# Kernel tuning notes

Measured on AMD Instinct MI355X. Metric: run time of the kernel, lower is better.

## Reference

```python
import jax, jax.numpy as jnp
import numpy as np

B, N = 32, 4096
EMBED_DIM = 256
D = H = W = 64


def setup_inputs() -> dict:
    key = jax.random.key(0)
    k1, k2, k3, k4 = jax.random.split(key, 4)
    points = jax.random.uniform(k1, (B, N, 3), dtype=jnp.float32) * D  # coords in [0, image_size)
    labels = jax.random.randint(k2, (B, N), 0, 2, dtype=jnp.int32)
    pos_embed = jax.random.normal(k3, (1, EMBED_DIM, D, H, W), dtype=jnp.float32) * 0.02
    point_emb = jax.random.normal(k4, (2, EMBED_DIM), dtype=jnp.float32)
    return {"points": points, "labels": labels, "pos_embed": pos_embed, "point_emb": point_emb}


def reference(points, labels, pos_embed, point_emb):
    # int() truncation (coords are non-negative) then clamp to grid bounds
    idx = jnp.clip(points.astype(jnp.int32), 0, jnp.array([D - 1, H - 1, W - 1], dtype=jnp.int32))
    zi, yi, xi = idx[..., 0], idx[..., 1], idx[..., 2]  # each [B, N]
    grid = jnp.transpose(pos_embed[0], (1, 2, 3, 0))  # [D, H, W, C]
    pos_enc = grid[zi, yi, xi]                        # [B, N, C] vectorized gather
    type_emb = point_emb[labels]                      # [B, N, C]
    return pos_enc + type_emb
```

## Files before the change

### kernel.cpp

```cpp
#include <hip/hip_runtime.h>


constexpr int B_ = 32;
constexpr int N_ = 4096;
constexpr int C_ = 256;
constexpr int GD = 64;
constexpr int PTS = B_ * N_;
constexpr int CELLS = GD * GD * GD;
constexpr int NBINS = GD * GD * (GD / 16);
constexpr int BPB = 8;
constexpr int NBLK = NBINS / BPB;
constexpr int TP = 260;

typedef float f32x4 __attribute__((ext_vector_type(4)));

__device__ __forceinline__ int clamp63(float v) {
    int i = (int)v;
    return min(max(i, 0), GD - 1);
}

__global__ __launch_bounds__(256) void k_zero(unsigned* __restrict__ hist) {
    int t = blockIdx.x * blockDim.x + threadIdx.x;
    if (t < NBINS) hist[t] = 0u;
}

__global__ __launch_bounds__(256) void k_hist(const float* __restrict__ points,
                                              unsigned* __restrict__ hist) {
    int p = blockIdx.x * blockDim.x + threadIdx.x;
    if (p >= PTS) return;
    int zi = clamp63(points[p * 3 + 0]);
    int yi = clamp63(points[p * 3 + 1]);
    int xi = clamp63(points[p * 3 + 2]);
    int key = (zi << 8) | (yi << 2) | (xi >> 4);
    atomicAdd(&hist[key], 1u);
}

__global__ __launch_bounds__(1024) void k_scan(const unsigned* __restrict__ hist,
                                               unsigned* __restrict__ cursor,
                                               unsigned* __restrict__ bin_ofs) {
    __shared__ unsigned sums[1024];
    const int t = threadIdx.x;
    unsigned h[16];
    unsigned s = 0;
    #pragma unroll
    for (int i = 0; i < 16; ++i) { h[i] = hist[t * 16 + i]; s += h[i]; }
    sums[t] = s;
    __syncthreads();
    for (int off = 1; off < 1024; off <<= 1) {
        unsigned v = (t >= off) ? sums[t - off] : 0u;
        __syncthreads();
        sums[t] += v;
        __syncthreads();
    }
    unsigned run = (t > 0) ? sums[t - 1] : 0u;
    #pragma unroll
    for (int i = 0; i < 16; ++i) {
        cursor[t * 16 + i]  = run;
        bin_ofs[t * 16 + i] = run;
        run += h[i];
    }
    if (t == 1023) bin_ofs[NBINS] = sums[1023];
}

__global__ __launch_bounds__(256) void k_scatter(const float* __restrict__ points,
                                                 const int* __restrict__ labels,
                                                 unsigned* __restrict__ cursor,
                                                 unsigned* __restrict__ recs) {
    int p = blockIdx.x * blockDim.x + threadIdx.x;
    if (p >= PTS) return;
    int zi = clamp63(points[p * 3 + 0]);
    int yi = clamp63(points[p * 3 + 1]);
    int xi = clamp63(points[p * 3 + 2]);
    int key = (zi << 8) | (yi << 2) | (xi >> 4);
    unsigned slot = atomicAdd(&cursor[key], 1u);
    recs[slot] = (unsigned)p | ((unsigned)labels[p] << 17) | ((unsigned)(xi & 15) << 18);
}

__global__ __launch_bounds__(256) void k_gather(const unsigned* __restrict__ bin_ofs,
                                                const unsigned* __restrict__ recs,
                                                const float* __restrict__ pos,
                                                const float* __restrict__ pemb,
                                                float* __restrict__ out) {
    __shared__ float tile[2][16 * TP];

    const int b    = blockIdx.x;
    const int swz  = (b & 7) * (NBLK >> 3) + (b >> 3);
    const int bin0 = swz * BPB;

    const int tid = threadIdx.x;
    const int w   = tid >> 6;
    const int l   = tid & 63;
    const int o4  = (tid & 3) << 2;
    const int csub = tid >> 2;

    const float4 te0 = *reinterpret_cast<const float4*>(pemb + 4 * l);
    const float4 te1 = *reinterpret_cast<const float4*>(pemb + C_ + 4 * l);

    auto linebase = [](int bin) -> size_t {
        return ((size_t)(bin >> 8) << 12) | ((size_t)((bin >> 2) & 63) << 6) |
               ((size_t)(bin & 3) << 4);
    };

    float4 rv0, rv1, rv2, rv3;
    {
        const size_t lb = linebase(bin0);
        rv0 = *reinterpret_cast<const float4*>(pos + (size_t)(  0 + csub) * CELLS + lb + o4);
        rv1 = *reinterpret_cast<const float4*>(pos + (size_t)( 64 + csub) * CELLS + lb + o4);
        rv2 = *reinterpret_cast<const float4*>(pos + (size_t)(128 + csub) * CELLS + lb + o4);
        rv3 = *reinterpret_cast<const float4*>(pos + (size_t)(192 + csub) * CELLS + lb + o4);
        float* t0 = tile[0];
        t0[(o4 + 0) * TP +   0 + csub] = rv0.x; t0[(o4 + 1) * TP +   0 + csub] = rv0.y;
        t0[(o4 + 2) * TP +   0 + csub] = rv0.z; t0[(o4 + 3) * TP +   0 + csub] = rv0.w;
        t0[(o4 + 0) * TP +  64 + csub] = rv1.x; t0[(o4 + 1) * TP +  64 + csub] = rv1.y;
        t0[(o4 + 2) * TP +  64 + csub] = rv1.z; t0[(o4 + 3) * TP +  64 + csub] = rv1.w;
        t0[(o4 + 0) * TP + 128 + csub] = rv2.x; t0[(o4 + 1) * TP + 128 + csub] = rv2.y;
        t0[(o4 + 2) * TP + 128 + csub] = rv2.z; t0[(o4 + 3) * TP + 128 + csub] = rv2.w;
        t0[(o4 + 0) * TP + 192 + csub] = rv3.x; t0[(o4 + 1) * TP + 192 + csub] = rv3.y;
        t0[(o4 + 2) * TP + 192 + csub] = rv3.z; t0[(o4 + 3) * TP + 192 + csub] = rv3.w;
    }

    for (int k = 0; k < BPB; ++k) {
        const int cur = k & 1;
        if (k + 1 < BPB) {
            const size_t lb = linebase(bin0 + k + 1);
            rv0 = *reinterpret_cast<const float4*>(pos + (size_t)(  0 + csub) * CELLS + lb + o4);
            rv1 = *reinterpret_cast<const float4*>(pos + (size_t)( 64 + csub) * CELLS + lb + o4);
            rv2 = *reinterpret_cast<const float4*>(pos + (size_t)(128 + csub) * CELLS + lb + o4);
            rv3 = *reinterpret_cast<const float4*>(pos + (size_t)(192 + csub) * CELLS + lb + o4);
        }
        __syncthreads();

        const int bin = bin0 + k;
        const unsigned start = bin_ofs[bin];
        const unsigned end   = bin_ofs[bin + 1];
        const float* tcur = tile[cur];
        for (unsigned i = start + w; i < end; i += 4) {
            const unsigned rec = recs[i];
            const unsigned p   = rec & 0x1FFFFu;
            const unsigned o   = rec >> 18;
            const float4 te = ((rec >> 17) & 1u) ? te1 : te0;
            const float4 v  = *reinterpret_cast<const float4*>(tcur + o * TP + 4 * l);
            f32x4 rr;
            rr.x = v.x + te.x; rr.y = v.y + te.y; rr.z = v.z + te.z; rr.w = v.w + te.w;
            __builtin_nontemporal_store(rr,
                reinterpret_cast<f32x4*>(out + (size_t)p * C_ + 4 * l));
        }

        if (k + 1 < BPB) {
            float* tn = tile[cur ^ 1];
            tn[(o4 + 0) * TP +   0 + csub] = rv0.x; tn[(o4 + 1) * TP +   0 + csub] = rv0.y;
            tn[(o4 + 2) * TP +   0 + csub] = rv0.z; tn[(o4 + 3) * TP +   0 + csub] = rv0.w;
            tn[(o4 + 0) * TP +  64 + csub] = rv1.x; tn[(o4 + 1) * TP +  64 + csub] = rv1.y;
            tn[(o4 + 2) * TP +  64 + csub] = rv1.z; tn[(o4 + 3) * TP +  64 + csub] = rv1.w;
            tn[(o4 + 0) * TP + 128 + csub] = rv2.x; tn[(o4 + 1) * TP + 128 + csub] = rv2.y;
            tn[(o4 + 2) * TP + 128 + csub] = rv2.z; tn[(o4 + 3) * TP + 128 + csub] = rv2.w;
            tn[(o4 + 0) * TP + 192 + csub] = rv3.x; tn[(o4 + 1) * TP + 192 + csub] = rv3.y;
            tn[(o4 + 2) * TP + 192 + csub] = rv3.z; tn[(o4 + 3) * TP + 192 + csub] = rv3.w;
        }
    }
}

__global__ __launch_bounds__(256) void k_naive(const float* __restrict__ points,
                                               const int* __restrict__ labels,
                                               const float* __restrict__ pos,
                                               const float* __restrict__ pemb,
                                               float* __restrict__ out) {
    const int t    = blockIdx.x * blockDim.x + threadIdx.x;
    const int p    = t >> 6;
    const int lane = t & 63;
    const int c4   = lane << 2;
    if (p >= PTS) return;
    int zi = clamp63(points[p * 3 + 0]);
    int yi = clamp63(points[p * 3 + 1]);
    int xi = clamp63(points[p * 3 + 2]);
    const int cell = (zi << 12) | (yi << 6) | xi;
    const int lab  = labels[p];
    const float4 te = *reinterpret_cast<const float4*>(pemb + lab * C_ + c4);
    const float* g = pos + cell;
    float4 r;
    r.x = g[(c4 + 0) * CELLS] + te.x;
    r.y = g[(c4 + 1) * CELLS] + te.y;
    r.z = g[(c4 + 2) * CELLS] + te.z;
    r.w = g[(c4 + 3) * CELLS] + te.w;
    *reinterpret_cast<float4*>(out + p * C_ + c4) = r;
}

extern "C" void kernel_launch(void* const* d_in, const int* in_sizes, int n_in,
                              void* d_out, int out_size, void* d_ws, size_t ws_size,
                              hipStream_t stream) {
    const float* points = (const float*)d_in[0];
    const int*   labels = (const int*)d_in[1];
    const float* pos    = (const float*)d_in[2];
    const float* pemb   = (const float*)d_in[3];
    float*       out    = (float*)d_out;

    const size_t need = (size_t)(NBINS * 3 + 1 + PTS) * sizeof(unsigned);
    if (ws_size < need) {
        const int total = PTS * 64;
        k_naive<<<(total + 255) / 256, 256, 0, stream>>>(points, labels, pos, pemb, out);
        return;
    }
    unsigned* hist    = (unsigned*)d_ws;
    unsigned* cursor  = hist + NBINS;
    unsigned* bin_ofs = cursor + NBINS;
    unsigned* recs    = bin_ofs + NBINS + 1;

    k_zero<<<(NBINS + 255) / 256, 256, 0, stream>>>(hist);
    k_hist<<<(PTS + 255) / 256, 256, 0, stream>>>(points, hist);
    k_scan<<<1, 1024, 0, stream>>>(hist, cursor, bin_ofs);
    k_scatter<<<(PTS + 255) / 256, 256, 0, stream>>>(points, labels, cursor, recs);
    k_gather<<<NBLK, 256, 0, stream>>>(bin_ofs, recs, pos, pemb, out);
}
```

Baseline: 108.8 us.

## Replace histogram+scan binning with fixed-capacity bins and overflow fallback

Drops the histogram, prefix-scan and second scatter pass, and bins points directly into fixed-capacity slots of 64 per bin with a single atomic pass. Points that overflow a bin are written directly by the scatter thread with a scalar per-channel loop. The zeroing kernel is replaced by a memset. This removes two kernel launches, the serial single-block scan and one full read of the points, at the cost of a larger, sparser record buffer. With the expected 2 points per bin on average, overflow should essentially never occur.

```diff
diff --git a/kernel.cpp b/kernel.cpp
--- a/kernel.cpp
+++ b/kernel.cpp
@@ -8,6 +8,7 @@
 constexpr int PTS = B_ * N_;
 constexpr int CELLS = GD * GD * GD;
 constexpr int NBINS = GD * GD * (GD / 16);
+constexpr int CAP = 64;
 constexpr int BPB = 8;
 constexpr int NBLK = NBINS / BPB;
 constexpr int TP = 260;
@@ -19,64 +20,32 @@
     return min(max(i, 0), GD - 1);
 }
 
-__global__ __launch_bounds__(256) void k_zero(unsigned* __restrict__ hist) {
-    int t = blockIdx.x * blockDim.x + threadIdx.x;
-    if (t < NBINS) hist[t] = 0u;
-}
-
-__global__ __launch_bounds__(256) void k_hist(const float* __restrict__ points,
-                                              unsigned* __restrict__ hist) {
+__global__ __launch_bounds__(256) void k_scatter(const float* __restrict__ points,
+                                                 const int* __restrict__ labels,
+                                                 unsigned* __restrict__ counts,
+                                                 unsigned* __restrict__ recs,
+                                                 const float* __restrict__ pos,
+                                                 const float* __restrict__ pemb,
+                                                 float* __restrict__ out) {
     int p = blockIdx.x * blockDim.x + threadIdx.x;
     if (p >= PTS) return;
     int zi = clamp63(points[p * 3 + 0]);
     int yi = clamp63(points[p * 3 + 1]);
     int xi = clamp63(points[p * 3 + 2]);
     int key = (zi << 8) | (yi << 2) | (xi >> 4);
-    atomicAdd(&hist[key], 1u);
+    int lab = labels[p];
+    unsigned slot = atomicAdd(&counts[key], 1u);
+    if (slot < CAP) {
+        recs[key * CAP + slot] =
+            (unsigned)p | ((unsigned)lab << 17) | ((unsigned)(xi & 15) << 18);
+    } else {
+        const int cell = (zi << 12) | (yi << 6) | xi;
+        for (int c = 0; c < C_; ++c)
+            out[(size_t)p * C_ + c] = pos[(size_t)c * CELLS + cell] + pemb[lab * C_ + c];
+    }
 }
 
-__global__ __launch_bounds__(1024) void k_scan(const unsigned* __restrict__ hist,
-                                               unsigned* __restrict__ cursor,
-                                               unsigned* __restrict__ bin_ofs) {
-    __shared__ unsigned sums[1024];
-    const int t = threadIdx.x;
-    unsigned h[16];
-    unsigned s = 0;
-    #pragma unroll
-    for (int i = 0; i < 16; ++i) { h[i] = hist[t * 16 + i]; s += h[i]; }
-    sums[t] = s;
-    __syncthreads();
-    for (int off = 1; off < 1024; off <<= 1) {
-        unsigned v = (t >= off) ? sums[t - off] : 0u;
-        __syncthreads();
-        sums[t] += v;
-        __syncthreads();
-    }
-    unsigned run = (t > 0) ? sums[t - 1] : 0u;
-    #pragma unroll
-    for (int i = 0; i < 16; ++i) {
-        cursor[t * 16 + i]  = run;
-        bin_ofs[t * 16 + i] = run;
-        run += h[i];
-    }
-    if (t == 1023) bin_ofs[NBINS] = sums[1023];
-}
-
-__global__ __launch_bounds__(256) void k_scatter(const float* __restrict__ points,
-                                                 const int* __restrict__ labels,
-                                                 unsigned* __restrict__ cursor,
-                                                 unsigned* __restrict__ recs) {
-    int p = blockIdx.x * blockDim.x + threadIdx.x;
-    if (p >= PTS) return;
-    int zi = clamp63(points[p * 3 + 0]);
-    int yi = clamp63(points[p * 3 + 1]);
-    int xi = clamp63(points[p * 3 + 2]);
-    int key = (zi << 8) | (yi << 2) | (xi >> 4);
-    unsigned slot = atomicAdd(&cursor[key], 1u);
-    recs[slot] = (unsigned)p | ((unsigned)labels[p] << 17) | ((unsigned)(xi & 15) << 18);
-}
-
-__global__ __launch_bounds__(256) void k_gather(const unsigned* __restrict__ bin_ofs,
+__global__ __launch_bounds__(256) void k_gather(const unsigned* __restrict__ counts,
                                                 const unsigned* __restrict__ recs,
                                                 const float* __restrict__ pos,
                                                 const float* __restrict__ pemb,
@@ -87,10 +56,10 @@
     const int swz  = (b & 7) * (NBLK >> 3) + (b >> 3);
     const int bin0 = swz * BPB;
 
-    const int tid = threadIdx.x;
-    const int w   = tid >> 6;
-    const int l   = tid & 63;
-    const int o4  = (tid & 3) << 2;
+    const int tid  = threadIdx.x;
+    const int w    = tid >> 6;
+    const int l    = tid & 63;
+    const int o4   = (tid & 3) << 2;
     const int csub = tid >> 2;
 
     const float4 te0 = *reinterpret_cast<const float4*>(pemb + 4 * l);
@@ -131,8 +100,9 @@
         __syncthreads();
 
         const int bin = bin0 + k;
-        const unsigned start = bin_ofs[bin];
-        const unsigned end   = bin_ofs[bin + 1];
+        const unsigned cnt   = min(counts[bin], (unsigned)CAP);
+        const unsigned start = (unsigned)bin * CAP;
+        const unsigned end   = start + cnt;
         const float* tcur = tile[cur];
         for (unsigned i = start + w; i < end; i += 4) {
             const unsigned rec = recs[i];
@@ -194,20 +164,17 @@
     const float* pemb   = (const float*)d_in[3];
     float*       out    = (float*)d_out;
 
-    const size_t need = (size_t)(NBINS * 3 + 1 + PTS) * sizeof(unsigned);
+    const size_t need = (size_t)(NBINS + NBINS * CAP) * sizeof(unsigned);
     if (ws_size < need) {
         const int total = PTS * 64;
         k_naive<<<(total + 255) / 256, 256, 0, stream>>>(points, labels, pos, pemb, out);
         return;
     }
-    unsigned* hist    = (unsigned*)d_ws;
-    unsigned* cursor  = hist + NBINS;
-    unsigned* bin_ofs = cursor + NBINS;
-    unsigned* recs    = bin_ofs + NBINS + 1;
+    unsigned* counts = (unsigned*)d_ws;
+    unsigned* recs   = counts + NBINS;
 
-    k_zero<<<(NBINS + 255) / 256, 256, 0, stream>>>(hist);
-    k_hist<<<(PTS + 255) / 256, 256, 0, stream>>>(points, hist);
-    k_scan<<<1, 1024, 0, stream>>>(hist, cursor, bin_ofs);
-    k_scatter<<<(PTS + 255) / 256, 256, 0, stream>>>(points, labels, cursor, recs);
-    k_gather<<<NBLK, 256, 0, stream>>>(bin_ofs, recs, pos, pemb, out);
+    hipMemsetAsync(counts, 0, NBINS * sizeof(unsigned), stream);
+    k_scatter<<<(PTS + 255) / 256, 256, 0, stream>>>(points, labels, counts, recs,
+                                                     pos, pemb, out);
+    k_gather<<<NBLK, 256, 0, stream>>>(counts, recs, pos, pemb, out);
 }
```

Result: faster. 97.91 us (-10.0%).
